# Kernel tuning notes

Hardware: AMD Instinct MI355X
Metric: run time of the kernel (lower is better)

## Reference

```python
import jax, jax.numpy as jnp
import numpy as np

B, IN, OUT, E, CTX, DEMO = 32768, 512, 128, 16, 256, 16
HID = IN // 2
GATE_IN = CTX + IN + DEMO  # 784


def setup_inputs() -> dict:
    key = jax.random.key(0)
    ks = jax.random.split(key, 9)
    inp = {
        'x': jax.random.normal(ks[0], (B, IN), dtype=jnp.float32),
        'u': jax.random.normal(ks[1], (B, CTX), dtype=jnp.float32),
        'd': jax.random.normal(ks[2], (B, DEMO), dtype=jnp.float32),
        # gate Linear(GATE_IN -> E)
        'gate_W': jax.random.normal(ks[3], (E, GATE_IN), dtype=jnp.float32) * 0.02,
        'gate_b': jnp.zeros((E,), dtype=jnp.float32),
        # per-expert MLP: Linear(IN->HID), ReLU, Linear(HID->OUT); stacked over experts
        'W1': jax.random.normal(ks[4], (E, HID, IN), dtype=jnp.float32) * 0.02,
        'b1': jnp.zeros((E, HID), dtype=jnp.float32),
        'W2': jax.random.normal(ks[5], (E, OUT, HID), dtype=jnp.float32) * 0.02,
        'b2': jnp.zeros((E, OUT), dtype=jnp.float32),
    }
    return inp


def reference(x, u, d, gate_W, gate_b, W1, b1, W2, b2):
    # gate input = cat([u, x, d], dim=1)  -> [B, GATE_IN]
    g_in = jnp.concatenate([u, x, d], axis=1)
    gate_logits = g_in @ gate_W.T + gate_b            # [B, E]
    weights = jax.nn.softmax(gate_logits, axis=1)     # [B, E]
    # all-expert MLP as batched GEMMs
    h = jax.nn.relu(jnp.einsum('bi,ehi->beh', x, W1) + b1[None])   # [B, E, HID]
    expert_outputs = jnp.einsum('beh,eoh->beo', h, W2) + b2[None]  # [B, E, OUT]
    # mixture_mode == 'logits': weighted sum over experts
    out = jnp.einsum('be,beo->bo', weights, expert_outputs)        # [B, OUT]
    return out
```

## Files before the change

kernel.cpp:

```cpp
#include <hip/hip_runtime.h>

#define B_    32768
#define IN_   512
#define HID_  256
#define OUT_  128
#define E_    16
#define CTX_  256
#define DEMO_ 16
#define GIN_  784

typedef __attribute__((ext_vector_type(8))) short short8;
typedef __attribute__((ext_vector_type(4))) float floatx4;

__device__ __forceinline__ short f2bf(float x){
  unsigned u = __builtin_bit_cast(unsigned, x);
  u += 0x7FFFu + ((u >> 16) & 1u);
  return (short)(u >> 16);
}

__device__ __forceinline__ short8 pack8(float4 a, float4 b){
  short8 r;
  r[0]=f2bf(a.x); r[1]=f2bf(a.y); r[2]=f2bf(a.z); r[3]=f2bf(a.w);
  r[4]=f2bf(b.x); r[5]=f2bf(b.y); r[6]=f2bf(b.z); r[7]=f2bf(b.w);
  return r;
}

__device__ __forceinline__ void load_lds16(const short* g, short* l){
  __builtin_amdgcn_global_load_lds((const __attribute__((address_space(1))) void*)g,
                                   (__attribute__((address_space(3))) void*)l,
                                   16, 0, 0);
}

__device__ __forceinline__ void stage128x64(short* lds, const short* g, int gpitch, int tid){
  const int wvv = tid >> 6, ln = tid & 63;
  const int cb = ln & 7, rsub = ln >> 3;
  #pragma unroll
  for (int i = 0; i < 4; ++i){
    const int r0  = (wvv*4 + i)*8;
    const int row = r0 + rsub;
    const short* gp = g + (size_t)row*gpitch + ((cb ^ rsub) << 3);
    load_lds16(gp, lds + r0*64);
  }
}

__global__ void convert_kernel(const float* __restrict__ x, const float* __restrict__ w1,
                               const float* __restrict__ w2, short* __restrict__ xb,
                               short* __restrict__ w1b, short* __restrict__ w2b){
  const int N1 = B_*IN_, N2 = E_*HID_*IN_, N3 = E_*OUT_*HID_;
  const int total4 = (N1 + N2 + N3) >> 2;
  for (int i = blockIdx.x*blockDim.x + threadIdx.x; i < total4; i += gridDim.x*blockDim.x){
    int e4 = i << 2;
    const float* src; short* dst; int off;
    if (e4 < N1)            { src = x;  dst = xb;  off = e4; }
    else if (e4 < N1 + N2)  { src = w1; dst = w1b; off = e4 - N1; }
    else                    { src = w2; dst = w2b; off = e4 - (N1 + N2); }
    float4 v = *(const float4*)(src + off);
    *(short4*)(dst + off) = make_short4(f2bf(v.x), f2bf(v.y), f2bf(v.z), f2bf(v.w));
  }
}

__global__ __launch_bounds__(256)
void gate_kernel(const float* __restrict__ u, const short* __restrict__ xb,
                 const float* __restrict__ d, const float* __restrict__ gW,
                 const float* __restrict__ gb, float* __restrict__ wout){
  const int tid  = threadIdx.x;
  const int wave = tid >> 6, lane = tid & 63;
  const int l15  = lane & 15, quad = lane >> 4;
  const int row0 = blockIdx.x*64 + wave*16;
  const int rA   = row0 + l15;
  const int kq   = quad*8;

  floatx4 acc  = {0.f,0.f,0.f,0.f};
  floatx4 acc2 = {0.f,0.f,0.f,0.f};

  #pragma unroll
  for (int t = 0; t < 8; ++t){
    const float4 a0 = *(const float4*)&u[(size_t)rA*CTX_ + t*32 + kq];
    const float4 a1 = *(const float4*)&u[(size_t)rA*CTX_ + t*32 + kq + 4];
    const float4 b0 = *(const float4*)&gW[(size_t)l15*GIN_ + t*32 + kq];
    const float4 b1 = *(const float4*)&gW[(size_t)l15*GIN_ + t*32 + kq + 4];
    acc = __builtin_amdgcn_mfma_f32_16x16x32_bf16(pack8(a0,a1), pack8(b0,b1), acc, 0,0,0);
  }
  #pragma unroll
  for (int t = 0; t < 16; ++t){
    const short8 af = *(const short8*)&xb[(size_t)rA*IN_ + t*32 + kq];
    const float4 b0 = *(const float4*)&gW[(size_t)l15*GIN_ + 256 + t*32 + kq];
    const float4 b1 = *(const float4*)&gW[(size_t)l15*GIN_ + 256 + t*32 + kq + 4];
    acc2 = __builtin_amdgcn_mfma_f32_16x16x32_bf16(af, pack8(b0,b1), acc2, 0,0,0);
  }
  {
    short8 af = {0,0,0,0,0,0,0,0}, bf = {0,0,0,0,0,0,0,0};
    if (quad < 2){
      const float4 a0 = *(const float4*)&d[(size_t)rA*DEMO_ + kq];
      const float4 a1 = *(const float4*)&d[(size_t)rA*DEMO_ + kq + 4];
      const float4 b0 = *(const float4*)&gW[(size_t)l15*GIN_ + 768 + kq];
      const float4 b1 = *(const float4*)&gW[(size_t)l15*GIN_ + 768 + kq + 4];
      af = pack8(a0,a1); bf = pack8(b0,b1);
    }
    acc = __builtin_amdgcn_mfma_f32_16x16x32_bf16(af, bf, acc, 0,0,0);
  }

  const float bias = gb[l15];
  #pragma unroll
  for (int r = 0; r < 4; ++r){
    float v = acc[r] + acc2[r] + bias;
    float m = v;
    #pragma unroll
    for (int s = 1; s <= 8; s <<= 1) m = fmaxf(m, __shfl_xor(m, s));
    const float p = __expf(v - m);
    float ssum = p;
    #pragma unroll
    for (int s = 1; s <= 8; s <<= 1) ssum += __shfl_xor(ssum, s);
    wout[(size_t)(row0 + quad*4 + r)*E_ + l15] = p / ssum;
  }
}

__global__ __launch_bounds__(256, 2)
void moe_kernel(const short* __restrict__ xb, const short* __restrict__ w1b,
                const short* __restrict__ w2b, const float* __restrict__ gatew,
                const float* __restrict__ b1g, const float* __restrict__ b2g,
                float* __restrict__ out){
  __shared__ alignas(16) char smem[51200];
  short* s_x  = (short*)smem;
  short* s_w1 = (short*)(smem + 16384);
  short* s_h  = (short*)smem;
  short* s_w2 = (short*)(smem + 34816);

  const int tid  = threadIdx.x;
  const int wv   = tid >> 6;
  const int lane = tid & 63;
  const int l15  = lane & 15;
  const int hi2  = lane >> 4;
  const int h_off  = (wv >> 1) * 64;
  const int mb_off = (wv & 1) * 64;
  const int m_off  = (wv >> 1) * 64;
  const int o_off  = (wv & 1) * 64;
  const int blk_m0 = blockIdx.x * 128;
  const int eg = blockIdx.y;

  floatx4 oacc[4][4];
  #pragma unroll
  for (int a = 0; a < 4; ++a)
    #pragma unroll
    for (int b = 0; b < 4; ++b) oacc[a][b] = floatx4{0.f,0.f,0.f,0.f};

  if (eg == 0){
    #pragma unroll 1
    for (int e = 0; e < E_; ++e){
      float b2v[4];
      #pragma unroll
      for (int nt = 0; nt < 4; ++nt) b2v[nt] = b2g[e*OUT_ + o_off + nt*16 + l15];
      #pragma unroll
      for (int mt = 0; mt < 4; ++mt){
        #pragma unroll
        for (int r = 0; r < 4; ++r){
          const float wgt = gatew[(size_t)(blk_m0 + m_off + mt*16 + hi2*4 + r)*E_ + e];
          #pragma unroll
          for (int nt = 0; nt < 4; ++nt) oacc[mt][nt][r] += wgt * b2v[nt];
        }
      }
    }
  }

  #pragma unroll 1
  for (int ei = 0; ei < 4; ++ei){
    const int e = eg*4 + ei;
    #pragma unroll 1
    for (int half = 0; half < 2; ++half){
      floatx4 g1[4][4];
      #pragma unroll
      for (int a = 0; a < 4; ++a)
        #pragma unroll
        for (int b = 0; b < 4; ++b) g1[a][b] = floatx4{0.f,0.f,0.f,0.f};

      const short* w1base = w1b + (size_t)(e*HID_ + half*128) * IN_;
      #pragma unroll 1
      for (int kc = 0; kc < 8; ++kc){
        stage128x64(s_x,  xb + (size_t)blk_m0*IN_ + kc*64, IN_, tid);
        stage128x64(s_w1, w1base + kc*64, IN_, tid);
        __syncthreads();
        #pragma unroll
        for (int ks = 0; ks < 2; ++ks){
          const int kb = ks*4 + hi2;
          const int sw = (kb ^ (l15 & 7)) << 3;
          short8 af[4], bf[4];
          #pragma unroll
          for (int ht = 0; ht < 4; ++ht)
            af[ht] = *(const short8*)&s_w1[(h_off + ht*16 + l15)*64 + sw];
          #pragma unroll
          for (int mt = 0; mt < 4; ++mt)
            bf[mt] = *(const short8*)&s_x[(mb_off + mt*16 + l15)*64 + sw];
          #pragma unroll
          for (int ht = 0; ht < 4; ++ht)
            #pragma unroll
            for (int mt = 0; mt < 4; ++mt)
              g1[ht][mt] = __builtin_amdgcn_mfma_f32_16x16x32_bf16(af[ht], bf[mt], g1[ht][mt], 0,0,0);
        }
        __syncthreads();
      }

      const short* w2base = w2b + (size_t)e*OUT_*HID_ + half*128;
      stage128x64(s_w2, w2base, HID_, tid);

      {
        float4 b1v[4];
        #pragma unroll
        for (int ht = 0; ht < 4; ++ht)
          b1v[ht] = *(const float4*)&b1g[e*HID_ + half*128 + h_off + ht*16 + hi2*4];
        float wgt[4];
        #pragma unroll
        for (int mt = 0; mt < 4; ++mt)
          wgt[mt] = gatew[(size_t)(blk_m0 + mb_off + mt*16 + l15)*E_ + e];
        #pragma unroll
        for (int ht = 0; ht < 4; ++ht){
          const float b1r[4] = {b1v[ht].x, b1v[ht].y, b1v[ht].z, b1v[ht].w};
          #pragma unroll
          for (int mt = 0; mt < 4; ++mt){
            short4 pk;
            float v0 = fmaxf(g1[ht][mt][0] + b1r[0], 0.f) * wgt[mt];
            float v1 = fmaxf(g1[ht][mt][1] + b1r[1], 0.f) * wgt[mt];
            float v2 = fmaxf(g1[ht][mt][2] + b1r[2], 0.f) * wgt[mt];
            float v3 = fmaxf(g1[ht][mt][3] + b1r[3], 0.f) * wgt[mt];
            pk.x = f2bf(v0); pk.y = f2bf(v1); pk.z = f2bf(v2); pk.w = f2bf(v3);
            *(short4*)&s_h[(size_t)(mb_off + mt*16 + l15)*136 + h_off + ht*16 + hi2*4] = pk;
          }
        }
      }
      __syncthreads();

      #pragma unroll 1
      for (int kc2 = 0; kc2 < 2; ++kc2){
        #pragma unroll
        for (int ks = 0; ks < 2; ++ks){
          const int kb = ks*4 + hi2;
          const int kk = kc2*64 + (kb << 3);
          const int sw = (kb ^ (l15 & 7)) << 3;
          short8 af[4], bf[4];
          #pragma unroll
          for (int mt = 0; mt < 4; ++mt)
            af[mt] = *(const short8*)&s_h[(m_off + mt*16 + l15)*136 + kk];
          #pragma unroll
          for (int nt = 0; nt < 4; ++nt)
            bf[nt] = *(const short8*)&s_w2[(o_off + nt*16 + l15)*64 + sw];
          #pragma unroll
          for (int mt = 0; mt < 4; ++mt)
            #pragma unroll
            for (int nt = 0; nt < 4; ++nt)
              oacc[mt][nt] = __builtin_amdgcn_mfma_f32_16x16x32_bf16(af[mt], bf[nt], oacc[mt][nt], 0,0,0);
        }
        __syncthreads();
        if (kc2 == 0){
          stage128x64(s_w2, w2base + 64, HID_, tid);
          __syncthreads();
        }
      }
    }
  }

  #pragma unroll
  for (int mt = 0; mt < 4; ++mt)
    #pragma unroll
    for (int nt = 0; nt < 4; ++nt)
      #pragma unroll
      for (int r = 0; r < 4; ++r)
        atomicAdd(&out[(size_t)(blk_m0 + m_off + mt*16 + hi2*4 + r)*OUT_ + o_off + nt*16 + l15],
                  oacc[mt][nt][r]);
}

extern "C" void kernel_launch(void* const* d_in, const int* in_sizes, int n_in,
                              void* d_out, int out_size, void* d_ws, size_t ws_size,
                              hipStream_t stream){
  const float* x  = (const float*)d_in[0];
  const float* u  = (const float*)d_in[1];
  const float* dd = (const float*)d_in[2];
  const float* gW = (const float*)d_in[3];
  const float* gb = (const float*)d_in[4];
  const float* W1 = (const float*)d_in[5];
  const float* b1 = (const float*)d_in[6];
  const float* W2 = (const float*)d_in[7];
  const float* b2 = (const float*)d_in[8];
  float* out = (float*)d_out;

  short* xb  = (short*)d_ws;
  short* w1b = xb  + (size_t)B_*IN_;
  short* w2b = w1b + (size_t)E_*HID_*IN_;
  float* gw  = (float*)(w2b + (size_t)E_*OUT_*HID_);

  hipMemsetAsync(d_out, 0, (size_t)B_*OUT_*sizeof(float), stream);
  hipLaunchKernelGGL(convert_kernel, dim3(4096), dim3(256), 0, stream, x, W1, W2, xb, w1b, w2b);
  hipLaunchKernelGGL(gate_kernel, dim3(B_/64), dim3(256), 0, stream, u, xb, dd, gW, gb, gw);
  hipLaunchKernelGGL(moe_kernel, dim3(B_/128, 4), dim3(256), 0, stream, xb, w1b, w2b, gw, b1, b2, out);
  (void)in_sizes; (void)n_in; (void)out_size; (void)ws_size;
}
```

Baseline: 379.8 us.

## Double-buffer LDS staging with 32-wide K chunks to overlap loads and MFMA

Both GEMM stages now stage 128x32 bf16 tiles into two alternating LDS buffers and issue the global-to-LDS copy for the next K chunk before computing on the current one. This replaces the load, barrier, compute, barrier pattern with one barrier per chunk. The aim is to hide global load latency behind MFMA work. The swizzle is reworked for the 32-wide row layout. The trade-off is twice as many K iterations and barriers per chunk of work, and smaller DMA transactions.

```diff
diff --git a/kernel.cpp b/kernel.cpp
--- a/kernel.cpp
+++ b/kernel.cpp
@@ -31,15 +31,15 @@
                                    16, 0, 0);
 }
 
-__device__ __forceinline__ void stage128x64(short* lds, const short* g, int gpitch, int tid){
+__device__ __forceinline__ void stage128x32(short* lds, const short* g, int gpitch, int tid){
   const int wvv = tid >> 6, ln = tid & 63;
-  const int cb = ln & 7, rsub = ln >> 3;
-  #pragma unroll
-  for (int i = 0; i < 4; ++i){
-    const int r0  = (wvv*4 + i)*8;
+  const int cb = ln & 3, rsub = ln >> 2;
+  #pragma unroll
+  for (int i = 0; i < 2; ++i){
+    const int r0  = (wvv*2 + i)*16;
     const int row = r0 + rsub;
-    const short* gp = g + (size_t)row*gpitch + ((cb ^ rsub) << 3);
-    load_lds16(gp, lds + r0*64);
+    const short* gp = g + (size_t)row*gpitch + ((cb ^ ((row >> 1) & 3)) << 3);
+    load_lds16(gp, lds + r0*32);
   }
 }
 
@@ -121,8 +121,6 @@
                 const float* __restrict__ b1g, const float* __restrict__ b2g,
                 float* __restrict__ out){
   __shared__ alignas(16) char smem[51200];
-  short* s_x  = (short*)smem;
-  short* s_w1 = (short*)(smem + 16384);
   short* s_h  = (short*)smem;
   short* s_w2 = (short*)(smem + 34816);
 
@@ -137,6 +135,7 @@
   const int o_off  = (wv & 1) * 64;
   const int blk_m0 = blockIdx.x * 128;
   const int eg = blockIdx.y;
+  const int sw = (hi2 ^ ((l15 >> 1) & 3)) << 3;
 
   floatx4 oacc[4][4];
   #pragma unroll
@@ -161,46 +160,51 @@
       }
     }
   }
+
+  const short* xbase = xb + (size_t)blk_m0*IN_;
 
   #pragma unroll 1
   for (int ei = 0; ei < 4; ++ei){
     const int e = eg*4 + ei;
     #pragma unroll 1
     for (int half = 0; half < 2; ++half){
+      const short* w1base = w1b + (size_t)(e*HID_ + half*128) * IN_;
+      const short* w2base = w2b + (size_t)e*OUT_*HID_ + half*128;
+
       floatx4 g1[4][4];
       #pragma unroll
       for (int a = 0; a < 4; ++a)
         #pragma unroll
         for (int b = 0; b < 4; ++b) g1[a][b] = floatx4{0.f,0.f,0.f,0.f};
 
-      const short* w1base = w1b + (size_t)(e*HID_ + half*128) * IN_;
+      stage128x32((short*)smem,          xbase,  IN_, tid);
+      stage128x32((short*)(smem + 8192), w1base, IN_, tid);
+      __syncthreads();
+
       #pragma unroll 1
-      for (int kc = 0; kc < 8; ++kc){
-        stage128x64(s_x,  xb + (size_t)blk_m0*IN_ + kc*64, IN_, tid);
-        stage128x64(s_w1, w1base + kc*64, IN_, tid);
+      for (int kc = 0; kc < 16; ++kc){
+        short* buf = (short*)(smem + (kc & 1)*16384);
+        if (kc < 15){
+          short* nbuf = (short*)(smem + ((kc + 1) & 1)*16384);
+          stage128x32(nbuf,        xbase  + (kc+1)*32, IN_, tid);
+          stage128x32(nbuf + 4096, w1base + (kc+1)*32, IN_, tid);
+        }
+        short8 af[4], bf[4];
+        #pragma unroll
+        for (int ht = 0; ht < 4; ++ht)
+          af[ht] = *(const short8*)&buf[4096 + (h_off + ht*16 + l15)*32 + sw];
+        #pragma unroll
+        for (int mt = 0; mt < 4; ++mt)
+          bf[mt] = *(const short8*)&buf[(mb_off + mt*16 + l15)*32 + sw];
+        #pragma unroll
+        for (int ht = 0; ht < 4; ++ht)
+          #pragma unroll
+          for (int mt = 0; mt < 4; ++mt)
+            g1[ht][mt] = __builtin_amdgcn_mfma_f32_16x16x32_bf16(af[ht], bf[mt], g1[ht][mt], 0,0,0);
         __syncthreads();
-        #pragma unroll
-        for (int ks = 0; ks < 2; ++ks){
-          const int kb = ks*4 + hi2;
-          const int sw = (kb ^ (l15 & 7)) << 3;
-          short8 af[4], bf[4];
-          #pragma unroll
-          for (int ht = 0; ht < 4; ++ht)
-            af[ht] = *(const short8*)&s_w1[(h_off + ht*16 + l15)*64 + sw];
-          #pragma unroll
-          for (int mt = 0; mt < 4; ++mt)
-            bf[mt] = *(const short8*)&s_x[(mb_off + mt*16 + l15)*64 + sw];
-          #pragma unroll
-          for (int ht = 0; ht < 4; ++ht)
-            #pragma unroll
-            for (int mt = 0; mt < 4; ++mt)
-              g1[ht][mt] = __builtin_amdgcn_mfma_f32_16x16x32_bf16(af[ht], bf[mt], g1[ht][mt], 0,0,0);
-        }
-        __syncthreads();
-      }
-
-      const short* w2base = w2b + (size_t)e*OUT_*HID_ + half*128;
-      stage128x64(s_w2, w2base, HID_, tid);
+      }
+
+      stage128x32(s_w2, w2base, HID_, tid);
 
       {
         float4 b1v[4];
@@ -229,30 +233,24 @@
       __syncthreads();
 
       #pragma unroll 1
-      for (int kc2 = 0; kc2 < 2; ++kc2){
-        #pragma unroll
-        for (int ks = 0; ks < 2; ++ks){
-          const int kb = ks*4 + hi2;
-          const int kk = kc2*64 + (kb << 3);
-          const int sw = (kb ^ (l15 & 7)) << 3;
-          short8 af[4], bf[4];
-          #pragma unroll
-          for (int mt = 0; mt < 4; ++mt)
-            af[mt] = *(const short8*)&s_h[(m_off + mt*16 + l15)*136 + kk];
+      for (int kc2 = 0; kc2 < 4; ++kc2){
+        if (kc2 < 3)
+          stage128x32(s_w2 + ((kc2 + 1) & 1)*4096, w2base + (kc2+1)*32, HID_, tid);
+        const short* wb = s_w2 + (kc2 & 1)*4096;
+        const int kk = kc2*32 + hi2*8;
+        short8 af[4], bf[4];
+        #pragma unroll
+        for (int mt = 0; mt < 4; ++mt)
+          af[mt] = *(const short8*)&s_h[(m_off + mt*16 + l15)*136 + kk];
+        #pragma unroll
+        for (int nt = 0; nt < 4; ++nt)
+          bf[nt] = *(const short8*)&wb[(o_off + nt*16 + l15)*32 + sw];
+        #pragma unroll
+        for (int mt = 0; mt < 4; ++mt)
           #pragma unroll
           for (int nt = 0; nt < 4; ++nt)
-            bf[nt] = *(const short8*)&s_w2[(o_off + nt*16 + l15)*64 + sw];
-          #pragma unroll
-          for (int mt = 0; mt < 4; ++mt)
-            #pragma unroll
-            for (int nt = 0; nt < 4; ++nt)
-              oacc[mt][nt] = __builtin_amdgcn_mfma_f32_16x16x32_bf16(af[mt], bf[nt], oacc[mt][nt], 0,0,0);
-        }
+            oacc[mt][nt] = __builtin_amdgcn_mfma_f32_16x16x32_bf16(af[mt], bf[nt], oacc[mt][nt], 0,0,0);
         __syncthreads();
-        if (kc2 == 0){
-          stage128x64(s_w2, w2base + 64, HID_, tid);
-          __syncthreads();
-        }
       }
     }
   }
```

After: 391.7 us. 1.03x slower.

## Double-buffer GEMM1 LDS staging and swizzle hidden tile to remove pipeline stalls

Applied to the files above, without the earlier changes.

Double-buffers the x/W1 tiles in LDS, so the async global-to-LDS load for the next K chunk is issued before computing the current one, and waits with explicit vmcnt counters and raw barriers. Both W2 halves are staged at once into a larger LDS region. The hidden-activation tile switches from padded pitch 136 to an XOR-swizzled pitch of 128. s_setprio is raised around the MFMA blocks. LDS grows to 64KB, which may limit occupancy to 2 blocks per CU as before, and the hand-written waitcnt logic is fragile.

```diff
diff --git a/kernel.cpp b/kernel.cpp
--- a/kernel.cpp
+++ b/kernel.cpp
@@ -30,6 +30,13 @@
                                    (__attribute__((address_space(3))) void*)l,
                                    16, 0, 0);
 }
+
+#define VMCNT8()  asm volatile("s_waitcnt vmcnt(8)"  ::: "memory")
+#define VMCNT0()  asm volatile("s_waitcnt vmcnt(0)"  ::: "memory")
+#define BAR() do{ asm volatile("" ::: "memory"); __builtin_amdgcn_s_barrier(); \
+                  asm volatile("" ::: "memory"); }while(0)
+#define LGKM0() do{ asm volatile("s_waitcnt lgkmcnt(0)" ::: "memory"); \
+                    __builtin_amdgcn_sched_barrier(0); }while(0)
 
 __device__ __forceinline__ void stage128x64(short* lds, const short* g, int gpitch, int tid){
   const int wvv = tid >> 6, ln = tid & 63;
@@ -120,17 +127,16 @@
                 const short* __restrict__ w2b, const float* __restrict__ gatew,
                 const float* __restrict__ b1g, const float* __restrict__ b2g,
                 float* __restrict__ out){
-  __shared__ alignas(16) char smem[51200];
-  short* s_x  = (short*)smem;
-  short* s_w1 = (short*)(smem + 16384);
+  __shared__ alignas(16) char smem[65536];
   short* s_h  = (short*)smem;
-  short* s_w2 = (short*)(smem + 34816);
+  short* s_w2 = (short*)(smem + 32768);
 
   const int tid  = threadIdx.x;
   const int wv   = tid >> 6;
   const int lane = tid & 63;
   const int l15  = lane & 15;
   const int hi2  = lane >> 4;
+  const int r7   = l15 & 7;
   const int h_off  = (wv >> 1) * 64;
   const int mb_off = (wv & 1) * 64;
   const int m_off  = (wv >> 1) * 64;
@@ -162,45 +168,62 @@
     }
   }
 
+  const short* xbase = xb + (size_t)blk_m0*IN_;
+
   #pragma unroll 1
   for (int ei = 0; ei < 4; ++ei){
     const int e = eg*4 + ei;
     #pragma unroll 1
     for (int half = 0; half < 2; ++half){
+      const short* w1base = w1b + (size_t)(e*HID_ + half*128) * IN_;
+      const short* w2base = w2b + (size_t)e*OUT_*HID_ + half*128;
+
       floatx4 g1[4][4];
       #pragma unroll
       for (int a = 0; a < 4; ++a)
         #pragma unroll
         for (int b = 0; b < 4; ++b) g1[a][b] = floatx4{0.f,0.f,0.f,0.f};
 
-      const short* w1base = w1b + (size_t)(e*HID_ + half*128) * IN_;
+      stage128x64((short*)(smem +      0), xbase,  IN_, tid);
+      stage128x64((short*)(smem + 16384), w1base, IN_, tid);
+
       #pragma unroll 1
       for (int kc = 0; kc < 8; ++kc){
-        stage128x64(s_x,  xb + (size_t)blk_m0*IN_ + kc*64, IN_, tid);
-        stage128x64(s_w1, w1base + kc*64, IN_, tid);
-        __syncthreads();
+        if (kc < 7){
+          char* nb = smem + ((kc + 1) & 1)*32768;
+          stage128x64((short*)nb,            xbase  + (kc+1)*64, IN_, tid);
+          stage128x64((short*)(nb + 16384),  w1base + (kc+1)*64, IN_, tid);
+          VMCNT8();
+        } else {
+          VMCNT0();
+        }
+        BAR();
+        const short* buf = (const short*)(smem + (kc & 1)*32768);
+        __builtin_amdgcn_s_setprio(1);
         #pragma unroll
         for (int ks = 0; ks < 2; ++ks){
-          const int kb = ks*4 + hi2;
-          const int sw = (kb ^ (l15 & 7)) << 3;
+          const int kb  = ks*4 + hi2;
+          const int swz = (kb ^ r7) << 3;
           short8 af[4], bf[4];
           #pragma unroll
           for (int ht = 0; ht < 4; ++ht)
-            af[ht] = *(const short8*)&s_w1[(h_off + ht*16 + l15)*64 + sw];
+            af[ht] = *(const short8*)&buf[8192 + (h_off + ht*16 + l15)*64 + swz];
           #pragma unroll
           for (int mt = 0; mt < 4; ++mt)
-            bf[mt] = *(const short8*)&s_x[(mb_off + mt*16 + l15)*64 + sw];
+            bf[mt] = *(const short8*)&buf[(mb_off + mt*16 + l15)*64 + swz];
           #pragma unroll
           for (int ht = 0; ht < 4; ++ht)
             #pragma unroll
             for (int mt = 0; mt < 4; ++mt)
               g1[ht][mt] = __builtin_amdgcn_mfma_f32_16x16x32_bf16(af[ht], bf[mt], g1[ht][mt], 0,0,0);
         }
-        __syncthreads();
+        __builtin_amdgcn_s_setprio(0);
+        LGKM0();
+        BAR();
       }
 
-      const short* w2base = w2b + (size_t)e*OUT_*HID_ + half*128;
-      stage128x64(s_w2, w2base, HID_, tid);
+      stage128x64(s_w2,        w2base,      HID_, tid);
+      stage128x64(s_w2 + 8192, w2base + 64, HID_, tid);
 
       {
         float4 b1v[4];
@@ -214,6 +237,7 @@
         #pragma unroll
         for (int ht = 0; ht < 4; ++ht){
           const float b1r[4] = {b1v[ht].x, b1v[ht].y, b1v[ht].z, b1v[ht].w};
+          const int hb3 = 2*ht + (hi2 >> 1);
           #pragma unroll
           for (int mt = 0; mt < 4; ++mt){
             short4 pk;
@@ -222,38 +246,40 @@
             float v2 = fmaxf(g1[ht][mt][2] + b1r[2], 0.f) * wgt[mt];
             float v3 = fmaxf(g1[ht][mt][3] + b1r[3], 0.f) * wgt[mt];
             pk.x = f2bf(v0); pk.y = f2bf(v1); pk.z = f2bf(v2); pk.w = f2bf(v3);
-            *(short4*)&s_h[(size_t)(mb_off + mt*16 + l15)*136 + h_off + ht*16 + hi2*4] = pk;
+            *(short4*)&s_h[(size_t)(mb_off + mt*16 + l15)*128 + h_off
+                           + ((hb3 ^ r7) << 3) + (hi2 & 1)*4] = pk;
           }
         }
       }
-      __syncthreads();
-
-      #pragma unroll 1
+      asm volatile("s_waitcnt vmcnt(0) lgkmcnt(0)" ::: "memory");
+      __builtin_amdgcn_sched_barrier(0);
+      BAR();
+
+      __builtin_amdgcn_s_setprio(1);
+      #pragma unroll
       for (int kc2 = 0; kc2 < 2; ++kc2){
+        const short* wb = s_w2 + kc2*8192;
         #pragma unroll
         for (int ks = 0; ks < 2; ++ks){
-          const int kb = ks*4 + hi2;
-          const int kk = kc2*64 + (kb << 3);
-          const int sw = (kb ^ (l15 & 7)) << 3;
+          const int kb  = ks*4 + hi2;
+          const int swz = (kb ^ r7) << 3;
           short8 af[4], bf[4];
           #pragma unroll
           for (int mt = 0; mt < 4; ++mt)
-            af[mt] = *(const short8*)&s_h[(m_off + mt*16 + l15)*136 + kk];
+            af[mt] = *(const short8*)&s_h[(size_t)(m_off + mt*16 + l15)*128 + kc2*64 + swz];
           #pragma unroll
           for (int nt = 0; nt < 4; ++nt)
-            bf[nt] = *(const short8*)&s_w2[(o_off + nt*16 + l15)*64 + sw];
+            bf[nt] = *(const short8*)&wb[(o_off + nt*16 + l15)*64 + swz];
           #pragma unroll
           for (int mt = 0; mt < 4; ++mt)
             #pragma unroll
             for (int nt = 0; nt < 4; ++nt)
               oacc[mt][nt] = __builtin_amdgcn_mfma_f32_16x16x32_bf16(af[mt], bf[nt], oacc[mt][nt], 0,0,0);
         }
-        __syncthreads();
-        if (kc2 == 0){
-          stage128x64(s_w2, w2base + 64, HID_, tid);
-          __syncthreads();
-        }
       }
+      __builtin_amdgcn_s_setprio(0);
+      LGKM0();
+      BAR();
     }
   }
 
```

After: 368.4 us. 1.03x faster.
